# Performance work log

Measured on AMD Instinct MI355X. Metric: run time of the kernel, lower is better.

Reference implementation:

```python
import jax, jax.numpy as jnp
import numpy as np

N = 100000   # nodes (single node type 'word')
R = 4        # relation types (sorted rel_names)
E = 160000   # edges per relation
H = 128      # h_dim
O = 64       # out_dim


def setup_inputs() -> dict:
    key = jax.random.key(0)
    k0, k1, k2, k3 = jax.random.split(key, 4)
    embed = jax.random.normal(k0, (N, H), jnp.float32) * 0.1          # RelGraphEmbed table
    weight = jax.random.normal(k1, (R, H, O), jnp.float32) / np.sqrt(H)  # layer-2 per-rel weight
    bias1 = jnp.zeros((H,), jnp.float32)   # layer-1 h_bias
    bias2 = jnp.zeros((O,), jnp.float32)   # layer-2 h_bias
    edge_src = jax.random.randint(k2, (R, E), 0, N)
    edge_dst = jax.random.randint(k3, (R, E), 0, N)
    return dict(embed=embed, weight=weight, bias1=bias1, bias2=bias2,
                edge_src=edge_src, edge_dst=edge_dst)


def _rel_mean(x, src, dst, num_nodes):
    # GraphConv(norm='right'): sum messages into dst, divide by dst in-degree.
    msg = x[src]                                                    # [E, d] gather
    summed = jax.ops.segment_sum(msg, dst, num_segments=num_nodes)  # scatter-add
    deg = jax.ops.segment_sum(jnp.ones(src.shape, x.dtype), dst, num_segments=num_nodes)
    return summed / jnp.maximum(deg, 1.0)[:, None]


def reference(embed, weight, bias1, bias2, edge_src, edge_dst):
    n = embed.shape[0]
    # Layer 1: weight=False -> HeteroGraphConv sums right-normalized aggregations, then bias+relu.
    h1 = jnp.zeros_like(embed)
    for r in range(edge_src.shape[0]):
        h1 = h1 + _rel_mean(embed, edge_src[r], edge_dst[r], n)
    h1 = jax.nn.relu(h1 + bias1)
    # Layer 2: per-relation linear transform, aggregate, sum over relations, bias (no activation).
    out = jnp.zeros((n, weight.shape[-1]), embed.dtype)
    for r in range(edge_src.shape[0]):
        out = out + _rel_mean(h1 @ weight[r], edge_src[r], edge_dst[r], n)
    return out + bias2
```

## Files before the change

kernel.cpp:

```cpp
#include <hip/hip_runtime.h>
#include <hip/hip_bf16.h>

#define H 128
#define O 64
#define RELS 4

typedef short short8 __attribute__((ext_vector_type(8)));
typedef float f32x4 __attribute__((ext_vector_type(4)));
typedef unsigned int u32x4 __attribute__((ext_vector_type(4)));

static __device__ __forceinline__ unsigned short f2b(float x) {
    __hip_bfloat16 h = __float2bfloat16(x);
    return *reinterpret_cast<unsigned short*>(&h);
}
static __device__ __forceinline__ float blo(unsigned u) { return __uint_as_float(u << 16); }
static __device__ __forceinline__ float bhi(unsigned u) { return __uint_as_float(u & 0xffff0000u); }

#define ACC8(acc, uv, wt)                                           \
    acc[0] += (wt) * blo(uv.x); acc[1] += (wt) * bhi(uv.x);         \
    acc[2] += (wt) * blo(uv.y); acc[3] += (wt) * bhi(uv.y);         \
    acc[4] += (wt) * blo(uv.z); acc[5] += (wt) * bhi(uv.z);         \
    acc[6] += (wt) * blo(uv.w); acc[7] += (wt) * bhi(uv.w);

__global__ void k_prep(const float* __restrict__ embed, unsigned short* __restrict__ eb,
                       const float* __restrict__ W, unsigned short* __restrict__ WT,
                       const int* __restrict__ dst, int* __restrict__ cnt,
                       int n4, int wtot, int E, int RE, int N, int b_h, int b_cvt) {
    int b = blockIdx.x;
    if (b < b_h) {
        int i = b * 256 + threadIdx.x;
        if (i < RE) { int r = i / E; atomicAdd(&cnt[r * N + dst[i]], 1); }
    } else if (b < b_h + b_cvt) {
        int base = (b - b_h) * 1024;
#pragma unroll
        for (int k = 0; k < 4; ++k) {
            int i = base + k * 256 + threadIdx.x;
            if (i < n4) {
                f32x4 v = __builtin_nontemporal_load(((const f32x4*)embed) + i);
                ushort4 o;
                o.x = f2b(v[0]); o.y = f2b(v[1]); o.z = f2b(v[2]); o.w = f2b(v[3]);
                ((ushort4*)eb)[i] = o;
            }
        }
    } else {
        int i = (b - b_h - b_cvt) * 256 + threadIdx.x;
        if (i < wtot) {
            int r = i >> 13;
            int n = (i >> 7) & (O - 1);
            int k = i & (H - 1);
            WT[i] = f2b(W[((size_t)r * H + k) * O + n]);
        }
    }
}

__global__ void k_scan1(const int* __restrict__ cnt, int* __restrict__ offs,
                        int* __restrict__ bsum, int n, int N_) {
    __shared__ int sh[256];
    int t = threadIdx.x;
    int base = blockIdx.x * 1024 + t * 4;
    int4 v = make_int4(0, 0, 0, 0);
    if (base + 3 < n && (N_ & 3) == 0) {
#pragma unroll
        for (int r = 0; r < RELS; ++r) {
            int4 c = *(const int4*)(cnt + (size_t)r * N_ + base);
            v.x += c.x; v.y += c.y; v.z += c.z; v.w += c.w;
        }
    } else {
        for (int j = 0; j < 4; ++j) {
            int i = base + j;
            if (i < n) {
                int s = 0;
                for (int r = 0; r < RELS; ++r) s += cnt[(size_t)r * N_ + i];
                (&v.x)[j] = s;
            }
        }
    }
    int s = v.x + v.y + v.z + v.w;
    sh[t] = s; __syncthreads();
    for (int off = 1; off < 256; off <<= 1) {
        int x = (t >= off) ? sh[t - off] : 0;
        __syncthreads();
        sh[t] += x;
        __syncthreads();
    }
    int incl = sh[t];
    int ex = incl - s;
    if (base < n)     offs[base]     = ex;
    if (base + 1 < n) offs[base + 1] = ex + v.x;
    if (base + 2 < n) offs[base + 2] = ex + v.x + v.y;
    if (base + 3 < n) offs[base + 3] = ex + v.x + v.y + v.z;
    if (t == 255) bsum[blockIdx.x] = incl;
}

__global__ void k_scan2(int* __restrict__ bsum, int nb) {
    __shared__ int sh[512];
    int t = threadIdx.x;
    int s = (t < nb) ? bsum[t] : 0;
    sh[t] = s; __syncthreads();
    for (int off = 1; off < 512; off <<= 1) {
        int x = (t >= off) ? sh[t - off] : 0;
        __syncthreads();
        sh[t] += x;
        __syncthreads();
    }
    if (t < nb) bsum[t] = sh[t] - s;
}

__global__ void k_scan3c(int* __restrict__ offs, const int* __restrict__ bsum,
                         const int* __restrict__ cnt, int* __restrict__ cursor,
                         int n, int total, int N_) {
    int i = blockIdx.x * blockDim.x + threadIdx.x;
    if (i < n) {
        int off = offs[i] + bsum[i >> 10];
        offs[i] = off;
        int c0 = cnt[i], c1 = cnt[N_ + i], c2 = cnt[2 * N_ + i];
        cursor[i]          = off;
        cursor[N_ + i]     = off + c0;
        cursor[2 * N_ + i] = off + c0 + c1;
        cursor[3 * N_ + i] = off + c0 + c1 + c2;
    }
    if (i == 0) offs[n] = total;
}

__global__ void k_fill(const int* __restrict__ src, const int* __restrict__ dst,
                       const int* __restrict__ cnt, int* __restrict__ cursor,
                       uint2* __restrict__ ue, int E, int RE, int N) {
    int i = blockIdx.x * blockDim.x + threadIdx.x;
    if (i >= RE) return;
    int r = i / E;
    int d = dst[i];
    int pos = atomicAdd(&cursor[r * N + d], 1);
    float w = 1.0f / (float)max(cnt[r * N + d], 1);
    ue[pos] = make_uint2((unsigned)(r * N + src[i]), __float_as_uint(w));
}

__global__ __launch_bounds__(256) void k_l1g(const unsigned short* __restrict__ eb,
                                             const int* __restrict__ offs2,
                                             const uint2* __restrict__ ue,
                                             const float* __restrict__ bias1,
                                             const unsigned short* __restrict__ WT,
                                             unsigned short* __restrict__ T, int N) {
    __shared__ __align__(16) unsigned short hs[16][136];
    __shared__ __align__(16) unsigned short st[4][16][72];
    int tid = threadIdx.x, wv = tid >> 6, l = tid & 63;
    int row0 = blockIdx.x * 16;
    int nloc = tid >> 4;
    int node = row0 + nloc;
    int q = l & 15;

    float a[8] = {0.f, 0.f, 0.f, 0.f, 0.f, 0.f, 0.f, 0.f};
    float c[8] = {0.f, 0.f, 0.f, 0.f, 0.f, 0.f, 0.f, 0.f};
    if (node < N) {
        int beg = offs2[node], end = offs2[node + 1];
        unsigned N1 = (unsigned)N, N2 = (unsigned)(2 * N);
        int e = beg;
        for (; e + 4 <= end; e += 4) {
            uint2 p0 = ue[e], p1 = ue[e + 1], p2 = ue[e + 2], p3 = ue[e + 3];
            unsigned s0 = p0.x; if (s0 >= N2) s0 -= N2; if (s0 >= N1) s0 -= N1;
            unsigned s1 = p1.x; if (s1 >= N2) s1 -= N2; if (s1 >= N1) s1 -= N1;
            unsigned s2 = p2.x; if (s2 >= N2) s2 -= N2; if (s2 >= N1) s2 -= N1;
            unsigned s3 = p3.x; if (s3 >= N2) s3 -= N2; if (s3 >= N1) s3 -= N1;
            float w0 = __uint_as_float(p0.y), w1 = __uint_as_float(p1.y);
            float w2 = __uint_as_float(p2.y), w3 = __uint_as_float(p3.y);
            uint4 u0 = *(const uint4*)(eb + (size_t)s0 * H + q * 8);
            uint4 u1 = *(const uint4*)(eb + (size_t)s1 * H + q * 8);
            uint4 u2 = *(const uint4*)(eb + (size_t)s2 * H + q * 8);
            uint4 u3 = *(const uint4*)(eb + (size_t)s3 * H + q * 8);
            ACC8(a, u0, w0);
            ACC8(c, u1, w1);
            ACC8(a, u2, w2);
            ACC8(c, u3, w3);
        }
        for (; e + 2 <= end; e += 2) {
            uint2 p0 = ue[e], p1 = ue[e + 1];
            unsigned s0 = p0.x; if (s0 >= N2) s0 -= N2; if (s0 >= N1) s0 -= N1;
            unsigned s1 = p1.x; if (s1 >= N2) s1 -= N2; if (s1 >= N1) s1 -= N1;
            float w0 = __uint_as_float(p0.y), w1 = __uint_as_float(p1.y);
            uint4 u0 = *(const uint4*)(eb + (size_t)s0 * H + q * 8);
            uint4 u1 = *(const uint4*)(eb + (size_t)s1 * H + q * 8);
            ACC8(a, u0, w0);
            ACC8(c, u1, w1);
        }
        if (e < end) {
            uint2 p0 = ue[e];
            unsigned s0 = p0.x; if (s0 >= N2) s0 -= N2; if (s0 >= N1) s0 -= N1;
            float w0 = __uint_as_float(p0.y);
            uint4 u0 = *(const uint4*)(eb + (size_t)s0 * H + q * 8);
            ACC8(a, u0, w0);
        }
        float4 b0 = *(const float4*)(bias1 + q * 8);
        float4 b1 = *(const float4*)(bias1 + q * 8 + 4);
        float f0 = fmaxf(a[0] + c[0] + b0.x, 0.f);
        float f1 = fmaxf(a[1] + c[1] + b0.y, 0.f);
        float f2 = fmaxf(a[2] + c[2] + b0.z, 0.f);
        float f3 = fmaxf(a[3] + c[3] + b0.w, 0.f);
        float f4 = fmaxf(a[4] + c[4] + b1.x, 0.f);
        float f5 = fmaxf(a[5] + c[5] + b1.y, 0.f);
        float f6 = fmaxf(a[6] + c[6] + b1.z, 0.f);
        float f7 = fmaxf(a[7] + c[7] + b1.w, 0.f);
        uint4 o;
        o.x = (unsigned)f2b(f0) | ((unsigned)f2b(f1) << 16);
        o.y = (unsigned)f2b(f2) | ((unsigned)f2b(f3) << 16);
        o.z = (unsigned)f2b(f4) | ((unsigned)f2b(f5) << 16);
        o.w = (unsigned)f2b(f6) | ((unsigned)f2b(f7) << 16);
        *(uint4*)&hs[nloc][q * 8] = o;
    } else {
        uint4 zz = make_uint4(0, 0, 0, 0);
        *(uint4*)&hs[nloc][q * 8] = zz;
    }
    __syncthreads();

    int rA = l & 15, kb = (l >> 4) * 8;
    short8 af[4];
#pragma unroll
    for (int kk = 0; kk < 4; ++kk)
        af[kk] = *(const short8*)&hs[rA][kk * 32 + kb];

    const unsigned short* Wb = WT + (size_t)wv * O * H;
    f32x4 z = {0.f, 0.f, 0.f, 0.f};
    f32x4 acc[4] = {z, z, z, z};
#pragma unroll
    for (int nt = 0; nt < 4; ++nt) {
        short8 bf[4];
#pragma unroll
        for (int kk = 0; kk < 4; ++kk)
            bf[kk] = *(const short8*)(Wb + ((size_t)(nt * 16 + rA)) * H + kk * 32 + kb);
#pragma unroll
        for (int kk = 0; kk < 4; ++kk)
            acc[nt] = __builtin_amdgcn_mfma_f32_16x16x32_bf16(af[kk], bf[kk], acc[nt], 0, 0, 0);
    }

#pragma unroll
    for (int nt = 0; nt < 4; ++nt)
#pragma unroll
        for (int j = 0; j < 4; ++j)
            st[wv][(l >> 4) * 4 + j][nt * 16 + rA] = f2b(acc[nt][j]);

#pragma unroll
    for (int i = 0; i < 2; ++i) {
        int rr = i * 8 + (l >> 3);
        u32x4 v = *(const u32x4*)&st[wv][rr][(l & 7) * 8];
        int grow = row0 + rr;
        if (grow < N)
            __builtin_nontemporal_store(v, (u32x4*)(T + ((size_t)wv * N + grow) * O + (l & 7) * 8));
    }
}

__global__ void k_pull2(const unsigned short* __restrict__ T, const int* __restrict__ offs2,
                        const uint2* __restrict__ ue, const float* __restrict__ bias2,
                        float* __restrict__ out, int N) {
    int node = blockIdx.x * 32 + (threadIdx.x >> 3);
    if (node >= N) return;
    int o = threadIdx.x & 7;
    int beg = offs2[node], end = offs2[node + 1];

    float a[8] = {0.f, 0.f, 0.f, 0.f, 0.f, 0.f, 0.f, 0.f};
    float c[8] = {0.f, 0.f, 0.f, 0.f, 0.f, 0.f, 0.f, 0.f};

    int e = beg;
    for (; e + 4 <= end; e += 4) {
        uint2 p0 = ue[e], p1 = ue[e + 1], p2 = ue[e + 2], p3 = ue[e + 3];
        float w0 = __uint_as_float(p0.y), w1 = __uint_as_float(p1.y);
        float w2 = __uint_as_float(p2.y), w3 = __uint_as_float(p3.y);
        uint4 u0 = *(const uint4*)(T + (size_t)p0.x * O + o * 8);
        uint4 u1 = *(const uint4*)(T + (size_t)p1.x * O + o * 8);
        uint4 u2 = *(const uint4*)(T + (size_t)p2.x * O + o * 8);
        uint4 u3 = *(const uint4*)(T + (size_t)p3.x * O + o * 8);
        ACC8(a, u0, w0);
        ACC8(c, u1, w1);
        ACC8(a, u2, w2);
        ACC8(c, u3, w3);
    }
    for (; e + 2 <= end; e += 2) {
        uint2 p0 = ue[e], p1 = ue[e + 1];
        float w0 = __uint_as_float(p0.y), w1 = __uint_as_float(p1.y);
        uint4 u0 = *(const uint4*)(T + (size_t)p0.x * O + o * 8);
        uint4 u1 = *(const uint4*)(T + (size_t)p1.x * O + o * 8);
        ACC8(a, u0, w0);
        ACC8(c, u1, w1);
    }
    if (e < end) {
        uint2 p0 = ue[e];
        float w0 = __uint_as_float(p0.y);
        uint4 u0 = *(const uint4*)(T + (size_t)p0.x * O + o * 8);
        ACC8(a, u0, w0);
    }

    float4 b0 = *(const float4*)(bias2 + o * 8);
    float4 b1 = *(const float4*)(bias2 + o * 8 + 4);
    f32x4 v0, v1;
    v0[0] = a[0] + c[0] + b0.x; v0[1] = a[1] + c[1] + b0.y;
    v0[2] = a[2] + c[2] + b0.z; v0[3] = a[3] + c[3] + b0.w;
    v1[0] = a[4] + c[4] + b1.x; v1[1] = a[5] + c[5] + b1.y;
    v1[2] = a[6] + c[6] + b1.z; v1[3] = a[7] + c[7] + b1.w;
    __builtin_nontemporal_store(v0, (f32x4*)(out + (size_t)node * O + o * 8));
    __builtin_nontemporal_store(v1, (f32x4*)(out + (size_t)node * O + o * 8 + 4));
}

extern "C" void kernel_launch(void* const* d_in, const int* in_sizes, int n_in,
                              void* d_out, int out_size, void* d_ws, size_t ws_size,
                              hipStream_t stream) {
    const float* embed  = (const float*)d_in[0];
    const float* weight = (const float*)d_in[1];
    const float* bias1  = (const float*)d_in[2];
    const float* bias2  = (const float*)d_in[3];
    const int*   esrc   = (const int*)d_in[4];
    const int*   edst   = (const int*)d_in[5];
    float* out = (float*)d_out;

    const int N = in_sizes[0] / H;
    const int E = in_sizes[4] / RELS;
    const int RN = RELS * N;
    const int RE = RELS * E;

    char* p = (char*)d_ws;
    auto alloc = [&](size_t bytes) {
        char* q = p;
        p += (bytes + 255) & ~(size_t)255;
        return q;
    };
    int* cnt    = (int*)alloc((size_t)RN * 4);
    int* offs2  = (int*)alloc(((size_t)N + 1) * 4);
    int* cursor = (int*)alloc((size_t)RN * 4);
    int* bsum   = (int*)alloc(4096);
    uint2* ue   = (uint2*)alloc((size_t)RE * 8);
    unsigned short* eb  = (unsigned short*)alloc((size_t)N * H * 2);
    unsigned short* WT  = (unsigned short*)alloc((size_t)RELS * O * H * 2);
    unsigned short* T   = (unsigned short*)alloc((size_t)RELS * N * O * 2);

    hipMemsetAsync(cnt, 0, (size_t)RN * 4, stream);

    int n4 = N * H / 4;
    int wtot = RELS * O * H;
    int b_h   = (RE + 255) / 256;
    int b_cvt = (n4 + 1023) / 1024;
    int b_w   = (wtot + 255) / 256;
    k_prep<<<b_h + b_cvt + b_w, 256, 0, stream>>>(embed, eb, weight, WT, edst, cnt,
                                                  n4, wtot, E, RE, N, b_h, b_cvt);

    int nb = (N + 1023) / 1024;
    k_scan1<<<nb, 256, 0, stream>>>(cnt, offs2, bsum, N, N);
    k_scan2<<<1, 512, 0, stream>>>(bsum, nb);
    k_scan3c<<<(N + 255) / 256, 256, 0, stream>>>(offs2, bsum, cnt, cursor, N, RE, N);

    k_fill<<<(RE + 255) / 256, 256, 0, stream>>>(esrc, edst, cnt, cursor, ue, E, RE, N);

    k_l1g<<<(N + 15) / 16, 256, 0, stream>>>(eb, offs2, ue, bias1, WT, T, N);

    k_pull2<<<(N + 31) / 32, 256, 0, stream>>>(T, offs2, ue, bias2, out, N);
}
```

Baseline: 182.2 us.

## Use persistent grid-stride blocks and hoist weight fragments into registers

Turns k_prep, k_fill, k_l1g and k_pull2 into grid-stride loops capped at 2048 blocks. In k_l1g, the per-wave bf16 weight fragments are loaded into registers once per block rather than once per tile, and the shared staging buffer is double-buffered so a block can loop over many tiles. The aim is to cut block launch overhead and repeated weight loads. In exchange, k_l1g holds 16 extra short8 values per thread, which raises register pressure and may lower occupancy for the latency-bound gathers.

```diff
diff --git a/kernel.cpp b/kernel.cpp
--- a/kernel.cpp
+++ b/kernel.cpp
@@ -25,30 +25,31 @@
 __global__ void k_prep(const float* __restrict__ embed, unsigned short* __restrict__ eb,
                        const float* __restrict__ W, unsigned short* __restrict__ WT,
                        const int* __restrict__ dst, int* __restrict__ cnt,
-                       int n4, int wtot, int E, int RE, int N, int b_h, int b_cvt) {
-    int b = blockIdx.x;
-    if (b < b_h) {
-        int i = b * 256 + threadIdx.x;
-        if (i < RE) { int r = i / E; atomicAdd(&cnt[r * N + dst[i]], 1); }
-    } else if (b < b_h + b_cvt) {
-        int base = (b - b_h) * 1024;
-#pragma unroll
-        for (int k = 0; k < 4; ++k) {
-            int i = base + k * 256 + threadIdx.x;
-            if (i < n4) {
-                f32x4 v = __builtin_nontemporal_load(((const f32x4*)embed) + i);
-                ushort4 o;
-                o.x = f2b(v[0]); o.y = f2b(v[1]); o.z = f2b(v[2]); o.w = f2b(v[3]);
-                ((ushort4*)eb)[i] = o;
-            }
-        }
-    } else {
-        int i = (b - b_h - b_cvt) * 256 + threadIdx.x;
-        if (i < wtot) {
-            int r = i >> 13;
-            int n = (i >> 7) & (O - 1);
-            int k = i & (H - 1);
-            WT[i] = f2b(W[((size_t)r * H + k) * O + n]);
+                       int n4, int wtot, int E, int RE, int N, int b_h, int b_cvt, int b_tot) {
+    for (int b = blockIdx.x; b < b_tot; b += gridDim.x) {
+        if (b < b_h) {
+            int i = b * 256 + threadIdx.x;
+            if (i < RE) { int r = i / E; atomicAdd(&cnt[r * N + dst[i]], 1); }
+        } else if (b < b_h + b_cvt) {
+            int base = (b - b_h) * 1024;
+#pragma unroll
+            for (int k = 0; k < 4; ++k) {
+                int i = base + k * 256 + threadIdx.x;
+                if (i < n4) {
+                    f32x4 v = __builtin_nontemporal_load(((const f32x4*)embed) + i);
+                    ushort4 o;
+                    o.x = f2b(v[0]); o.y = f2b(v[1]); o.z = f2b(v[2]); o.w = f2b(v[3]);
+                    ((ushort4*)eb)[i] = o;
+                }
+            }
+        } else {
+            int i = (b - b_h - b_cvt) * 256 + threadIdx.x;
+            if (i < wtot) {
+                int r = i >> 13;
+                int n = (i >> 7) & (O - 1);
+                int k = i & (H - 1);
+                WT[i] = f2b(W[((size_t)r * H + k) * O + n]);
+            }
         }
     }
 }
@@ -125,13 +126,13 @@
 __global__ void k_fill(const int* __restrict__ src, const int* __restrict__ dst,
                        const int* __restrict__ cnt, int* __restrict__ cursor,
                        uint2* __restrict__ ue, int E, int RE, int N) {
-    int i = blockIdx.x * blockDim.x + threadIdx.x;
-    if (i >= RE) return;
-    int r = i / E;
-    int d = dst[i];
-    int pos = atomicAdd(&cursor[r * N + d], 1);
-    float w = 1.0f / (float)max(cnt[r * N + d], 1);
-    ue[pos] = make_uint2((unsigned)(r * N + src[i]), __float_as_uint(w));
+    for (int i = blockIdx.x * blockDim.x + threadIdx.x; i < RE; i += gridDim.x * blockDim.x) {
+        int r = i / E;
+        int d = dst[i];
+        int pos = atomicAdd(&cursor[r * N + d], 1);
+        float w = 1.0f / (float)max(cnt[r * N + d], 1);
+        ue[pos] = make_uint2((unsigned)(r * N + src[i]), __float_as_uint(w));
+    }
 }
 
 __global__ __launch_bounds__(256) void k_l1g(const unsigned short* __restrict__ eb,
@@ -139,33 +140,146 @@
                                              const uint2* __restrict__ ue,
                                              const float* __restrict__ bias1,
                                              const unsigned short* __restrict__ WT,
-                                             unsigned short* __restrict__ T, int N) {
-    __shared__ __align__(16) unsigned short hs[16][136];
+                                             unsigned short* __restrict__ T,
+                                             int N, int ntiles) {
+    __shared__ __align__(16) unsigned short hs[2][16][136];
     __shared__ __align__(16) unsigned short st[4][16][72];
     int tid = threadIdx.x, wv = tid >> 6, l = tid & 63;
-    int row0 = blockIdx.x * 16;
     int nloc = tid >> 4;
-    int node = row0 + nloc;
     int q = l & 15;
-
-    float a[8] = {0.f, 0.f, 0.f, 0.f, 0.f, 0.f, 0.f, 0.f};
-    float c[8] = {0.f, 0.f, 0.f, 0.f, 0.f, 0.f, 0.f, 0.f};
-    if (node < N) {
-        int beg = offs2[node], end = offs2[node + 1];
-        unsigned N1 = (unsigned)N, N2 = (unsigned)(2 * N);
+    int rA = l & 15, kb = (l >> 4) * 8;
+    unsigned N1 = (unsigned)N, N2 = (unsigned)(2 * N);
+
+    float4 b0 = *(const float4*)(bias1 + q * 8);
+    float4 b1 = *(const float4*)(bias1 + q * 8 + 4);
+    const unsigned short* Wb = WT + (size_t)wv * O * H;
+    short8 bf[4][4];
+#pragma unroll
+    for (int nt = 0; nt < 4; ++nt)
+#pragma unroll
+        for (int kk = 0; kk < 4; ++kk)
+            bf[nt][kk] = *(const short8*)(Wb + ((size_t)(nt * 16 + rA)) * H + kk * 32 + kb);
+
+    int buf = 0;
+    for (int tile = blockIdx.x; tile < ntiles; tile += gridDim.x, buf ^= 1) {
+        int row0 = tile * 16;
+        int node = row0 + nloc;
+
+        float a[8] = {0.f, 0.f, 0.f, 0.f, 0.f, 0.f, 0.f, 0.f};
+        float c[8] = {0.f, 0.f, 0.f, 0.f, 0.f, 0.f, 0.f, 0.f};
+        if (node < N) {
+            int2 be = *(const int2*)(offs2 + node);
+            int beg = be.x, end = be.y;
+            int e = beg;
+            for (; e + 4 <= end; e += 4) {
+                uint2 p0 = ue[e], p1 = ue[e + 1], p2 = ue[e + 2], p3 = ue[e + 3];
+                unsigned s0 = p0.x; if (s0 >= N2) s0 -= N2; if (s0 >= N1) s0 -= N1;
+                unsigned s1 = p1.x; if (s1 >= N2) s1 -= N2; if (s1 >= N1) s1 -= N1;
+                unsigned s2 = p2.x; if (s2 >= N2) s2 -= N2; if (s2 >= N1) s2 -= N1;
+                unsigned s3 = p3.x; if (s3 >= N2) s3 -= N2; if (s3 >= N1) s3 -= N1;
+                float w0 = __uint_as_float(p0.y), w1 = __uint_as_float(p1.y);
+                float w2 = __uint_as_float(p2.y), w3 = __uint_as_float(p3.y);
+                uint4 u0 = *(const uint4*)(eb + (size_t)s0 * H + q * 8);
+                uint4 u1 = *(const uint4*)(eb + (size_t)s1 * H + q * 8);
+                uint4 u2 = *(const uint4*)(eb + (size_t)s2 * H + q * 8);
+                uint4 u3 = *(const uint4*)(eb + (size_t)s3 * H + q * 8);
+                ACC8(a, u0, w0);
+                ACC8(c, u1, w1);
+                ACC8(a, u2, w2);
+                ACC8(c, u3, w3);
+            }
+            for (; e + 2 <= end; e += 2) {
+                uint2 p0 = ue[e], p1 = ue[e + 1];
+                unsigned s0 = p0.x; if (s0 >= N2) s0 -= N2; if (s0 >= N1) s0 -= N1;
+                unsigned s1 = p1.x; if (s1 >= N2) s1 -= N2; if (s1 >= N1) s1 -= N1;
+                float w0 = __uint_as_float(p0.y), w1 = __uint_as_float(p1.y);
+                uint4 u0 = *(const uint4*)(eb + (size_t)s0 * H + q * 8);
+                uint4 u1 = *(const uint4*)(eb + (size_t)s1 * H + q * 8);
+                ACC8(a, u0, w0);
+                ACC8(c, u1, w1);
+            }
+            if (e < end) {
+                uint2 p0 = ue[e];
+                unsigned s0 = p0.x; if (s0 >= N2) s0 -= N2; if (s0 >= N1) s0 -= N1;
+                float w0 = __uint_as_float(p0.y);
+                uint4 u0 = *(const uint4*)(eb + (size_t)s0 * H + q * 8);
+                ACC8(a, u0, w0);
+            }
+            float f0 = fmaxf(a[0] + c[0] + b0.x, 0.f);
+            float f1 = fmaxf(a[1] + c[1] + b0.y, 0.f);
+            float f2 = fmaxf(a[2] + c[2] + b0.z, 0.f);
+            float f3 = fmaxf(a[3] + c[3] + b0.w, 0.f);
+            float f4 = fmaxf(a[4] + c[4] + b1.x, 0.f);
+            float f5 = fmaxf(a[5] + c[5] + b1.y, 0.f);
+            float f6 = fmaxf(a[6] + c[6] + b1.z, 0.f);
+            float f7 = fmaxf(a[7] + c[7] + b1.w, 0.f);
+            uint4 o;
+            o.x = (unsigned)f2b(f0) | ((unsigned)f2b(f1) << 16);
+            o.y = (unsigned)f2b(f2) | ((unsigned)f2b(f3) << 16);
+            o.z = (unsigned)f2b(f4) | ((unsigned)f2b(f5) << 16);
+            o.w = (unsigned)f2b(f6) | ((unsigned)f2b(f7) << 16);
+            *(uint4*)&hs[buf][nloc][q * 8] = o;
+        } else {
+            uint4 zz = make_uint4(0, 0, 0, 0);
+            *(uint4*)&hs[buf][nloc][q * 8] = zz;
+        }
+        __syncthreads();
+
+        short8 af[4];
+#pragma unroll
+        for (int kk = 0; kk < 4; ++kk)
+            af[kk] = *(const short8*)&hs[buf][rA][kk * 32 + kb];
+
+        f32x4 z = {0.f, 0.f, 0.f, 0.f};
+        f32x4 acc[4] = {z, z, z, z};
+#pragma unroll
+        for (int nt = 0; nt < 4; ++nt)
+#pragma unroll
+            for (int kk = 0; kk < 4; ++kk)
+                acc[nt] = __builtin_amdgcn_mfma_f32_16x16x32_bf16(af[kk], bf[nt][kk], acc[nt], 0, 0, 0);
+
+#pragma unroll
+        for (int nt = 0; nt < 4; ++nt)
+#pragma unroll
+            for (int j = 0; j < 4; ++j)
+                st[wv][(l >> 4) * 4 + j][nt * 16 + rA] = f2b(acc[nt][j]);
+
+#pragma unroll
+        for (int i = 0; i < 2; ++i) {
+            int rr = i * 8 + (l >> 3);
+            u32x4 v = *(const u32x4*)&st[wv][rr][(l & 7) * 8];
+            int grow = row0 + rr;
+            if (grow < N)
+                __builtin_nontemporal_store(v, (u32x4*)(T + ((size_t)wv * N + grow) * O + (l & 7) * 8));
+        }
+    }
+}
+
+__global__ void k_pull2(const unsigned short* __restrict__ T, const int* __restrict__ offs2,
+                        const uint2* __restrict__ ue, const float* __restrict__ bias2,
+                        float* __restrict__ out, int N, int ngroups) {
+    int o = threadIdx.x & 7;
+    float4 b0 = *(const float4*)(bias2 + o * 8);
+    float4 b1 = *(const float4*)(bias2 + o * 8 + 4);
+
+    for (int g = blockIdx.x; g < ngroups; g += gridDim.x) {
+        int node = g * 32 + (threadIdx.x >> 3);
+        if (node >= N) continue;
+        int2 be = *(const int2*)(offs2 + node);
+        int beg = be.x, end = be.y;
+
+        float a[8] = {0.f, 0.f, 0.f, 0.f, 0.f, 0.f, 0.f, 0.f};
+        float c[8] = {0.f, 0.f, 0.f, 0.f, 0.f, 0.f, 0.f, 0.f};
+
         int e = beg;
         for (; e + 4 <= end; e += 4) {
             uint2 p0 = ue[e], p1 = ue[e + 1], p2 = ue[e + 2], p3 = ue[e + 3];
-            unsigned s0 = p0.x; if (s0 >= N2) s0 -= N2; if (s0 >= N1) s0 -= N1;
-            unsigned s1 = p1.x; if (s1 >= N2) s1 -= N2; if (s1 >= N1) s1 -= N1;
-            unsigned s2 = p2.x; if (s2 >= N2) s2 -= N2; if (s2 >= N1) s2 -= N1;
-            unsigned s3 = p3.x; if (s3 >= N2) s3 -= N2; if (s3 >= N1) s3 -= N1;
             float w0 = __uint_as_float(p0.y), w1 = __uint_as_float(p1.y);
             float w2 = __uint_as_float(p2.y), w3 = __uint_as_float(p3.y);
-            uint4 u0 = *(const uint4*)(eb + (size_t)s0 * H + q * 8);
-            uint4 u1 = *(const uint4*)(eb + (size_t)s1 * H + q * 8);
-            uint4 u2 = *(const uint4*)(eb + (size_t)s2 * H + q * 8);
-            uint4 u3 = *(const uint4*)(eb + (size_t)s3 * H + q * 8);
+            uint4 u0 = *(const uint4*)(T + (size_t)p0.x * O + o * 8);
+            uint4 u1 = *(const uint4*)(T + (size_t)p1.x * O + o * 8);
+            uint4 u2 = *(const uint4*)(T + (size_t)p2.x * O + o * 8);
+            uint4 u3 = *(const uint4*)(T + (size_t)p3.x * O + o * 8);
             ACC8(a, u0, w0);
             ACC8(c, u1, w1);
             ACC8(a, u2, w2);
@@ -173,128 +287,27 @@
         }
         for (; e + 2 <= end; e += 2) {
             uint2 p0 = ue[e], p1 = ue[e + 1];
-            unsigned s0 = p0.x; if (s0 >= N2) s0 -= N2; if (s0 >= N1) s0 -= N1;
-            unsigned s1 = p1.x; if (s1 >= N2) s1 -= N2; if (s1 >= N1) s1 -= N1;
             float w0 = __uint_as_float(p0.y), w1 = __uint_as_float(p1.y);
-            uint4 u0 = *(const uint4*)(eb + (size_t)s0 * H + q * 8);
-            uint4 u1 = *(const uint4*)(eb + (size_t)s1 * H + q * 8);
+            uint4 u0 = *(const uint4*)(T + (size_t)p0.x * O + o * 8);
+            uint4 u1 = *(const uint4*)(T + (size_t)p1.x * O + o * 8);
             ACC8(a, u0, w0);
             ACC8(c, u1, w1);
         }
         if (e < end) {
             uint2 p0 = ue[e];
-            unsigned s0 = p0.x; if (s0 >= N2) s0 -= N2; if (s0 >= N1) s0 -= N1;
             float w0 = __uint_as_float(p0.y);
-            uint4 u0 = *(const uint4*)(eb + (size_t)s0 * H + q * 8);
+            uint4 u0 = *(const uint4*)(T + (size_t)p0.x * O + o * 8);
             ACC8(a, u0, w0);
         }
-        float4 b0 = *(const float4*)(bias1 + q * 8);
-        float4 b1 = *(const float4*)(bias1 + q * 8 + 4);
-        float f0 = fmaxf(a[0] + c[0] + b0.x, 0.f);
-        float f1 = fmaxf(a[1] + c[1] + b0.y, 0.f);
-        float f2 = fmaxf(a[2] + c[2] + b0.z, 0.f);
-        float f3 = fmaxf(a[3] + c[3] + b0.w, 0.f);
-        float f4 = fmaxf(a[4] + c[4] + b1.x, 0.f);
-        float f5 = fmaxf(a[5] + c[5] + b1.y, 0.f);
-        float f6 = fmaxf(a[6] + c[6] + b1.z, 0.f);
-        float f7 = fmaxf(a[7] + c[7] + b1.w, 0.f);
-        uint4 o;
-        o.x = (unsigned)f2b(f0) | ((unsigned)f2b(f1) << 16);
-        o.y = (unsigned)f2b(f2) | ((unsigned)f2b(f3) << 16);
-        o.z = (unsigned)f2b(f4) | ((unsigned)f2b(f5) << 16);
-        o.w = (unsigned)f2b(f6) | ((unsigned)f2b(f7) << 16);
-        *(uint4*)&hs[nloc][q * 8] = o;
-    } else {
-        uint4 zz = make_uint4(0, 0, 0, 0);
-        *(uint4*)&hs[nloc][q * 8] = zz;
-    }
-    __syncthreads();
-
-    int rA = l & 15, kb = (l >> 4) * 8;
-    short8 af[4];
-#pragma unroll
-    for (int kk = 0; kk < 4; ++kk)
-        af[kk] = *(const short8*)&hs[rA][kk * 32 + kb];
-
-    const unsigned short* Wb = WT + (size_t)wv * O * H;
-    f32x4 z = {0.f, 0.f, 0.f, 0.f};
-    f32x4 acc[4] = {z, z, z, z};
-#pragma unroll
-    for (int nt = 0; nt < 4; ++nt) {
-        short8 bf[4];
-#pragma unroll
-        for (int kk = 0; kk < 4; ++kk)
-            bf[kk] = *(const short8*)(Wb + ((size_t)(nt * 16 + rA)) * H + kk * 32 + kb);
-#pragma unroll
-        for (int kk = 0; kk < 4; ++kk)
-            acc[nt] = __builtin_amdgcn_mfma_f32_16x16x32_bf16(af[kk], bf[kk], acc[nt], 0, 0, 0);
-    }
-
-#pragma unroll
-    for (int nt = 0; nt < 4; ++nt)
-#pragma unroll
-        for (int j = 0; j < 4; ++j)
-            st[wv][(l >> 4) * 4 + j][nt * 16 + rA] = f2b(acc[nt][j]);
-
-#pragma unroll
-    for (int i = 0; i < 2; ++i) {
-        int rr = i * 8 + (l >> 3);
-        u32x4 v = *(const u32x4*)&st[wv][rr][(l & 7) * 8];
-        int grow = row0 + rr;
-        if (grow < N)
-            __builtin_nontemporal_store(v, (u32x4*)(T + ((size_t)wv * N + grow) * O + (l & 7) * 8));
-    }
-}
-
-__global__ void k_pull2(const unsigned short* __restrict__ T, const int* __restrict__ offs2,
-                        const uint2* __restrict__ ue, const float* __restrict__ bias2,
-                        float* __restrict__ out, int N) {
-    int node = blockIdx.x * 32 + (threadIdx.x >> 3);
-    if (node >= N) return;
-    int o = threadIdx.x & 7;
-    int beg = offs2[node], end = offs2[node + 1];
-
-    float a[8] = {0.f, 0.f, 0.f, 0.f, 0.f, 0.f, 0.f, 0.f};
-    float c[8] = {0.f, 0.f, 0.f, 0.f, 0.f, 0.f, 0.f, 0.f};
-
-    int e = beg;
-    for (; e + 4 <= end; e += 4) {
-        uint2 p0 = ue[e], p1 = ue[e + 1], p2 = ue[e + 2], p3 = ue[e + 3];
-        float w0 = __uint_as_float(p0.y), w1 = __uint_as_float(p1.y);
-        float w2 = __uint_as_float(p2.y), w3 = __uint_as_float(p3.y);
-        uint4 u0 = *(const uint4*)(T + (size_t)p0.x * O + o * 8);
-        uint4 u1 = *(const uint4*)(T + (size_t)p1.x * O + o * 8);
-        uint4 u2 = *(const uint4*)(T + (size_t)p2.x * O + o * 8);
-        uint4 u3 = *(const uint4*)(T + (size_t)p3.x * O + o * 8);
-        ACC8(a, u0, w0);
-        ACC8(c, u1, w1);
-        ACC8(a, u2, w2);
-        ACC8(c, u3, w3);
-    }
-    for (; e + 2 <= end; e += 2) {
-        uint2 p0 = ue[e], p1 = ue[e + 1];
-        float w0 = __uint_as_float(p0.y), w1 = __uint_as_float(p1.y);
-        uint4 u0 = *(const uint4*)(T + (size_t)p0.x * O + o * 8);
-        uint4 u1 = *(const uint4*)(T + (size_t)p1.x * O + o * 8);
-        ACC8(a, u0, w0);
-        ACC8(c, u1, w1);
-    }
-    if (e < end) {
-        uint2 p0 = ue[e];
-        float w0 = __uint_as_float(p0.y);
-        uint4 u0 = *(const uint4*)(T + (size_t)p0.x * O + o * 8);
-        ACC8(a, u0, w0);
-    }
-
-    float4 b0 = *(const float4*)(bias2 + o * 8);
-    float4 b1 = *(const float4*)(bias2 + o * 8 + 4);
-    f32x4 v0, v1;
-    v0[0] = a[0] + c[0] + b0.x; v0[1] = a[1] + c[1] + b0.y;
-    v0[2] = a[2] + c[2] + b0.z; v0[3] = a[3] + c[3] + b0.w;
-    v1[0] = a[4] + c[4] + b1.x; v1[1] = a[5] + c[5] + b1.y;
-    v1[2] = a[6] + c[6] + b1.z; v1[3] = a[7] + c[7] + b1.w;
-    __builtin_nontemporal_store(v0, (f32x4*)(out + (size_t)node * O + o * 8));
-    __builtin_nontemporal_store(v1, (f32x4*)(out + (size_t)node * O + o * 8 + 4));
+
+        f32x4 v0, v1;
+        v0[0] = a[0] + c[0] + b0.x; v0[1] = a[1] + c[1] + b0.y;
+        v0[2] = a[2] + c[2] + b0.z; v0[3] = a[3] + c[3] + b0.w;
+        v1[0] = a[4] + c[4] + b1.x; v1[1] = a[5] + c[5] + b1.y;
+        v1[2] = a[6] + c[6] + b1.z; v1[3] = a[7] + c[7] + b1.w;
+        __builtin_nontemporal_store(v0, (f32x4*)(out + (size_t)node * O + o * 8));
+        __builtin_nontemporal_store(v1, (f32x4*)(out + (size_t)node * O + o * 8 + 4));
+    }
 }
 
 extern "C" void kernel_launch(void* const* d_in, const int* in_sizes, int n_in,
@@ -335,17 +348,22 @@
     int b_h   = (RE + 255) / 256;
     int b_cvt = (n4 + 1023) / 1024;
     int b_w   = (wtot + 255) / 256;
-    k_prep<<<b_h + b_cvt + b_w, 256, 0, stream>>>(embed, eb, weight, WT, edst, cnt,
-                                                  n4, wtot, E, RE, N, b_h, b_cvt);
+    int b_tot = b_h + b_cvt + b_w;
+    int gprep = b_tot < 2048 ? b_tot : 2048;
+    k_prep<<<gprep, 256, 0, stream>>>(embed, eb, weight, WT, edst, cnt,
+                                      n4, wtot, E, RE, N, b_h, b_cvt, b_tot);
 
     int nb = (N + 1023) / 1024;
     k_scan1<<<nb, 256, 0, stream>>>(cnt, offs2, bsum, N, N);
     k_scan2<<<1, 512, 0, stream>>>(bsum, nb);
     k_scan3c<<<(N + 255) / 256, 256, 0, stream>>>(offs2, bsum, cnt, cursor, N, RE, N);
 
-    k_fill<<<(RE + 255) / 256, 256, 0, stream>>>(esrc, edst, cnt, cursor, ue, E, RE, N);
-
-    k_l1g<<<(N + 15) / 16, 256, 0, stream>>>(eb, offs2, ue, bias1, WT, T, N);
-
-    k_pull2<<<(N + 31) / 32, 256, 0, stream>>>(T, offs2, ue, bias2, out, N);
-}
+    int bfill = (RE + 255) / 256;
+    k_fill<<<(bfill < 2048 ? bfill : 2048), 256, 0, stream>>>(esrc, edst, cnt, cursor, ue, E, RE, N);
+
+    int ntiles = (N + 15) / 16;
+    k_l1g<<<(ntiles < 2048 ? ntiles : 2048), 256, 0, stream>>>(eb, offs2, ue, bias1, WT, T, N, ntiles);
+
+    int ngroups = (N + 31) / 32;
+    k_pull2<<<(ngroups < 2048 ? ngroups : 2048), 256, 0, stream>>>(T, offs2, ue, bias2, out, N, ngroups);
+}
```

Result: faster. 170.5 us (-6.4%).
